# Kernel optimization log

Hardware: AMD Instinct MI355X
Metric: run time of the kernel (lower is better)

The kernel has to match this reference:

```python
import jax, jax.numpy as jnp
import numpy as np
from itertools import permutations

D_DIA, L_DIA, N_DIM, NHID, NUM_K = 128, 40, 512, 512, 4
N_UTT = D_DIA * L_DIA          # 5120 utterances
N_NODE = 3 * N_UTT             # 15360 graph nodes (l,a,v per utterance)


def _build_edges(n_dia, dia_l):
    """Replicates create_gnn_index edge construction for uniform dialogue length.
    Intra-modal: all ordered pairs within each modality block per dialogue.
    Cross-modal: ordered pairs among {l_t, a_t, v_t} for each utterance t."""
    base = (np.arange(n_dia) * 3 * dia_l).reshape(n_dia, 1, 1)
    p, q = np.meshgrid(np.arange(dia_l), np.arange(dia_l), indexing='ij')
    mask = p != q
    pp, qq = p[mask], q[mask]                      # [L*(L-1)]
    moff = (np.arange(3) * dia_l).reshape(1, 3, 1)  # modality block offsets
    src_i = (base + moff + pp.reshape(1, 1, -1)).ravel()
    dst_i = (base + moff + qq.reshape(1, 1, -1)).ravel()
    tri = np.array(list(permutations(range(3), 2)))  # [6,2]
    t = np.arange(dia_l).reshape(1, 1, -1)
    src_c = (base + tri[:, 0].reshape(1, 6, 1) * dia_l + t).ravel()
    dst_c = (base + tri[:, 1].reshape(1, 6, 1) * dia_l + t).ravel()
    src = np.concatenate([src_i, src_c]).astype(np.int32)
    dst = np.concatenate([dst_i, dst_c]).astype(np.int32)
    return jnp.asarray(src), jnp.asarray(dst)


def setup_inputs() -> dict:
    key = jax.random.key(0)
    ks = jax.random.split(key, 10)
    a = jax.random.normal(ks[0], (N_UTT, N_DIM), jnp.float32)
    v = jax.random.normal(ks[1], (N_UTT, N_DIM), jnp.float32)
    l = jax.random.normal(ks[2], (N_UTT, N_DIM), jnp.float32)
    qmask = jax.random.uniform(ks[3], (L_DIA, D_DIA, 2), jnp.float32)
    dia_len = jnp.full((D_DIA,), L_DIA, jnp.int32)
    spk_emb = jax.random.normal(ks[4], (2, N_DIM), jnp.float32)
    fc1_W = jax.random.normal(ks[5], (N_DIM, NHID), jnp.float32) / np.sqrt(N_DIM)
    fc1_b = jnp.zeros((NHID,), jnp.float32)
    convW = jax.random.normal(ks[6], (NUM_K, NHID, NHID), jnp.float32) / np.sqrt(NHID)
    convb = jnp.zeros((NUM_K, NHID), jnp.float32)
    src, dst = _build_edges(D_DIA, L_DIA)
    return {"a": a, "v": v, "l": l, "qmask": qmask, "spk_emb": spk_emb,
            "fc1_W": fc1_W, "fc1_b": fc1_b, "convW": convW, "convb": convb,
            "dia_len": dia_len, "epoch": 0, "src": src, "dst": dst}


def _gcn_conv(x, src, dst, W, b):
    # GCNConv: D^{-1/2}(A+I)D^{-1/2} X W + b, scatter-add aggregation over edges
    n = x.shape[0]
    deg = jax.ops.segment_sum(jnp.ones(src.shape[0], x.dtype), dst, num_segments=n) + 1.0
    norm = jax.lax.rsqrt(deg)
    coef = norm[src] * norm[dst]                       # [E]
    agg = jax.ops.segment_sum(x[src] * coef[:, None], dst, num_segments=n)
    agg = agg + x / deg[:, None]                       # self-loop term
    return agg @ W + b


def reference(a, v, l, qmask, spk_emb, fc1_W, fc1_b, convW, convb, dia_len, epoch, src, dst):
    n_dia = dia_len.shape[0]
    ll = L_DIA
    # speaker embedding added to text modality (use_speaker=True, 'l' in modals)
    spk_idx = jnp.argmax(qmask[:ll].transpose(1, 0, 2).reshape(-1, qmask.shape[-1]), axis=-1)
    l = l + spk_emb[spk_idx]
    # node features ordered per dialogue as [l_block, a_block, v_block]
    feats = jnp.concatenate([l.reshape(n_dia, ll, -1),
                             a.reshape(n_dia, ll, -1),
                             v.reshape(n_dia, ll, -1)], axis=1).reshape(3 * n_dia * ll, -1)
    x1 = feats @ fc1_W + fc1_b
    gnn_out = x1
    for k in range(convW.shape[0]):
        gnn_out = gnn_out + _gcn_conv(gnn_out, src, dst, convW[k], convb[k])
    out2 = jnp.concatenate([x1, gnn_out], axis=1)
    out2 = jnp.concatenate([feats, out2], axis=-1)     # use_residue=True
    # reverse_features: regroup per dialogue, concat modalities on feature dim
    d2 = out2.shape[-1]
    r = out2.reshape(n_dia, 3, ll, d2)
    out1 = jnp.concatenate([r[:, 0], r[:, 1], r[:, 2]], axis=-1).reshape(n_dia * ll, 3 * d2)
    return out1
```

## Files before the change

kernel.cpp:

```cpp
#include <hip/hip_runtime.h>
#include <cstdint>
#include <cstddef>

typedef unsigned short u16;
typedef __attribute__((ext_vector_type(8))) short bf16x8;
typedef __attribute__((ext_vector_type(4))) float f32x4;

__device__ __forceinline__ float b2f(u16 u) {
  union { uint32_t i; float f; } x; x.i = ((uint32_t)u) << 16; return x.f;
}
__device__ __forceinline__ u16 f2b(float f) {
  union { float f; uint32_t i; } x; x.f = f;
  uint32_t u = x.i;
  u += 0x7fffu + ((u >> 16) & 1u);
  return (u16)(u >> 16);
}
__device__ __forceinline__ void load8(const void* p, size_t idx, bool f32, float o[8]) {
  if (f32) {
    const float4* fp = (const float4*)((const float*)p + idx);
    float4 x = fp[0], y = fp[1];
    o[0] = x.x; o[1] = x.y; o[2] = x.z; o[3] = x.w;
    o[4] = y.x; o[5] = y.y; o[6] = y.z; o[7] = y.w;
  } else {
    uint4 w = *(const uint4*)((const u16*)p + idx);
    uint32_t ww[4] = {w.x, w.y, w.z, w.w};
#pragma unroll
    for (int q = 0; q < 4; q++) {
      o[2 * q]     = b2f((u16)(ww[q] & 0xffffu));
      o[2 * q + 1] = b2f((u16)(ww[q] >> 16));
    }
  }
}
__device__ __forceinline__ void store8_bf16(u16* p, size_t idx, const float o[8]) {
  uint32_t w[4];
#pragma unroll
  for (int q = 0; q < 4; q++)
    w[q] = (uint32_t)f2b(o[2 * q]) | ((uint32_t)f2b(o[2 * q + 1]) << 16);
  *(uint4*)(p + idx) = make_uint4(w[0], w[1], w[2], w[3]);
}

__device__ __forceinline__ bool detect_f32(const u16* lb, int* ldsflag, int tid) {
  if (tid < 64) {
    int bad = 0;
    for (int i = tid; i < 1024; i += 64) {
      float f = b2f(lb[i]);
      if (!(fabsf(f) <= 1.0e4f)) bad = 1;
    }
    int any = __any(bad);
    if (tid == 0) *ldsflag = any;
  }
  __syncthreads();
  const bool r = (*ldsflag != 0);
  __syncthreads();
  return r;
}


__global__ __launch_bounds__(1024)
void transw_k(const void* __restrict__ fc1W, const void* __restrict__ convW,
              const u16* __restrict__ lbits, u16* __restrict__ WtF)
{
  __shared__ u16 tile[32][33];
  __shared__ int flagS;
  const int tx = threadIdx.x, ty = threadIdx.y;
  const int tid = ty * 32 + tx;
  const bool f32 = detect_f32(lbits, &flagS, tid);
  const int w = blockIdx.z;
  const void* W = (w == 0) ? fc1W : convW;
  const size_t base = (w == 0) ? 0 : (size_t)(w - 1) * 262144;
  const int bx = blockIdx.x, by = blockIdx.y;
  const size_t i = base + (size_t)(by * 32 + ty) * 512 + (bx * 32 + tx);
  float val = f32 ? ((const float*)W)[i] : b2f(((const u16*)W)[i]);
  tile[ty][tx] = f2b(val);
  __syncthreads();
  const int e = tid & 7, l16 = (tid >> 3) & 15, q = (tid >> 7) & 3, nbp = tid >> 9;
  const u16 vv = tile[q * 8 + e][nbp * 16 + l16];
  WtF[(size_t)w * 262144 + ((size_t)((bx * 2 + nbp) * 16 + by)) * 512 +
      (q * 16 + l16) * 8 + e] = vv;
}


__device__ __forceinline__ void gemm_layer(f32x4 (&acc)[8][4], const u16* Xs,
                                           const u16* __restrict__ WL,
                                           int nt, int lane)
{
  const int lane8 = lane * 8;
  bf16x8 cw[4], nw[4];
#pragma unroll
  for (int nb = 0; nb < 4; ++nb)
    cw[nb] = *(const bf16x8*)(WL + (((nt * 4 + nb) * 16) << 9) + lane8);
#pragma unroll 2
  for (int kb = 0; kb < 16; ++kb) {
    if (kb < 15) {
#pragma unroll
      for (int nb = 0; nb < 4; ++nb)
        nw[nb] = *(const bf16x8*)(WL + (((nt * 4 + nb) * 16 + kb + 1) << 9) + lane8);
    }
    bf16x8 af[4];
#pragma unroll
    for (int rb = 0; rb < 4; ++rb)
      af[rb] = *(const bf16x8*)&Xs[((rb * 16 + kb) << 9) + lane8];
    __builtin_amdgcn_s_setprio(1);
#pragma unroll
    for (int rb = 0; rb < 4; ++rb)
#pragma unroll
      for (int nb = 0; nb < 4; ++nb)
        acc[rb][nb] = __builtin_amdgcn_mfma_f32_16x16x32_bf16(af[rb], cw[nb],
                                                              acc[rb][nb], 0, 0, 0);
    __builtin_amdgcn_s_setprio(0);
#pragma unroll
    for (int rb = 4; rb < 8; ++rb)
      af[rb - 4] = *(const bf16x8*)&Xs[((rb * 16 + kb) << 9) + lane8];
    __builtin_amdgcn_s_setprio(1);
#pragma unroll
    for (int rb = 4; rb < 8; ++rb)
#pragma unroll
      for (int nb = 0; nb < 4; ++nb)
        acc[rb][nb] = __builtin_amdgcn_mfma_f32_16x16x32_bf16(af[rb - 4], cw[nb],
                                                              acc[rb][nb], 0, 0, 0);
    __builtin_amdgcn_s_setprio(0);
#pragma unroll
    for (int nb = 0; nb < 4; ++nb) cw[nb] = nw[nb];
  }
}

__device__ __forceinline__ void bias_add(f32x4 (&acc)[8][4], const void* bptr,
                                         int boff, bool f32io, int nt, int l16)
{
#pragma unroll
  for (int nb = 0; nb < 4; ++nb) {
    const int col = nt * 64 + nb * 16 + l16;
    const float b = f32io ? ((const float*)bptr)[boff + col]
                          : b2f(((const u16*)bptr)[boff + col]);
#pragma unroll
    for (int rb = 0; rb < 8; ++rb)
#pragma unroll
      for (int r = 0; r < 4; ++r) acc[rb][nb][r] += b;
  }
}

__device__ __forceinline__ void writeout_co(void* outv, const f32x4 (&acc)[8][4],
                                            float* S, int d, int cbase, bool f32io,
                                            int nt, int quad, int l16, int tid)
{
  const int rg = tid >> 6;
  const int cs = (tid & 63) * 8;
#pragma unroll
  for (int p = 0; p < 3; ++p) {
    const int p0 = p * 40;
    __syncthreads();
#pragma unroll
    for (int rb = 0; rb < 8; ++rb)
#pragma unroll
      for (int r = 0; r < 4; ++r) {
        const int row = rb * 16 + quad * 4 + r;
        const int lr = row - p0;
        if (lr >= 0 && lr < 40) {
#pragma unroll
          for (int nb = 0; nb < 4; ++nb)
            S[lr * 516 + nt * 64 + nb * 16 + l16] = acc[rb][nb][r];
        }
      }
    __syncthreads();
#pragma unroll
    for (int it = 0; it < 5; ++it) {
      const int lr = it * 8 + rg;
      const size_t ob = (size_t)(d * 40 + lr) * 4608 + (size_t)p * 1536 + cbase + cs;
      const float* sp = &S[lr * 516 + cs];
      if (f32io) {
        float4 v0 = *(const float4*)sp, v1 = *(const float4*)(sp + 4);
        float* op = (float*)outv + ob;
        *(float4*)op = v0; *(float4*)(op + 4) = v1;
      } else {
        float vals[8];
#pragma unroll
        for (int q2 = 0; q2 < 8; ++q2) vals[q2] = sp[q2];
        store8_bf16((u16*)outv, ob, vals);
      }
    }
  }
}

__device__ __forceinline__ void gb_agg(const f32x4 (&acc)[8][4], u16* Xs,
                                       int nt, int lane, int quad, int l16)
{
#pragma unroll
  for (int nb = 0; nb < 4; ++nb) {
    const int c = nt * 64 + nb * 16 + l16;
    const int kc = c >> 5, cq = (c >> 3) & 3, e = c & 7;
#pragma unroll
    for (int rb = 0; rb < 8; ++rb)
#pragma unroll
      for (int r = 0; r < 4; ++r) {
        const int row = rb * 16 + quad * 4 + r;
        if (row < 120)
          Xs[((rb * 16 + kc) << 9) + (cq * 16 + (row & 15)) * 8 + e] =
              f2b(acc[rb][nb][r]);
      }
  }
  asm volatile("s_waitcnt lgkmcnt(0)" ::: "memory");
  const int c = nt * 64 + lane;
  const int kc = c >> 5, cq = (c >> 3) & 3, e = c & 7;
  float bs[3];
#pragma unroll
  for (int m = 0; m < 3; ++m) {
    float s = 0.f;
#pragma unroll 8
    for (int t = 0; t < 40; ++t) {
      const int row = m * 40 + t;
      s += b2f(Xs[(((row >> 4) * 16 + kc) << 9) + (cq * 16 + (row & 15)) * 8 + e]);
    }
    bs[m] = s;
  }
  const float inv42 = 1.0f / 42.0f;
#pragma unroll 4
  for (int t = 0; t < 40; ++t) {
    const int r0 = t, r1 = 40 + t, r2 = 80 + t;
    const int i0 = (((r0 >> 4) * 16 + kc) << 9) + (cq * 16 + (r0 & 15)) * 8 + e;
    const int i1 = (((r1 >> 4) * 16 + kc) << 9) + (cq * 16 + (r1 & 15)) * 8 + e;
    const int i2 = (((r2 >> 4) * 16 + kc) << 9) + (cq * 16 + (r2 & 15)) * 8 + e;
    const float x0 = b2f(Xs[i0]), x1 = b2f(Xs[i1]), x2 = b2f(Xs[i2]);
    Xs[i0] = f2b((bs[0] + x1 + x2) * inv42);
    Xs[i1] = f2b((bs[1] + x0 + x2) * inv42);
    Xs[i2] = f2b((bs[2] + x0 + x1) * inv42);
  }
}

__global__ __launch_bounds__(512, 2)
void fused_k(const void* __restrict__ a, const void* __restrict__ v,
             const void* __restrict__ l, const void* __restrict__ qmask,
             const void* __restrict__ spk, const void* __restrict__ fc1b,
             const void* __restrict__ convb, const u16* __restrict__ WtF,
             void* __restrict__ outv)
{
  __shared__ __align__(16) u16 Xs[65536];
  __shared__ int flagS;
  const int tid = threadIdx.x;
  const bool f32io = detect_f32((const u16*)l, &flagS, tid);
  const int d = blockIdx.x;
  const int lane = tid & 63, nt = tid >> 6;
  const int quad = lane >> 4, l16 = lane & 15;

  {
    const int cs = (tid & 63) * 8;
    const int rg = tid >> 6;
    const int kc = cs >> 5, cq = (cs >> 3) & 3;
#pragma unroll
    for (int it = 0; it < 15; ++it) {
      const int r = it * 8 + rg;
      const int mod = r / 40, t = r - mod * 40;
      const int u = d * 40 + t;
      float vals[8];
      const void* srcp = (mod == 1) ? a : ((mod == 2) ? v : l);
      load8(srcp, (size_t)u * 512 + cs, f32io, vals);
      if (mod == 0) {
        const int qi = (t * 128 + d) * 2;
        float q0 = f32io ? ((const float*)qmask)[qi]     : b2f(((const u16*)qmask)[qi]);
        float q1 = f32io ? ((const float*)qmask)[qi + 1] : b2f(((const u16*)qmask)[qi + 1]);
        const int sidx = (q1 > q0) ? 1 : 0;
        float sv[8];
        load8(spk, (size_t)sidx * 512 + cs, f32io, sv);
#pragma unroll
        for (int j = 0; j < 8; ++j) vals[j] += sv[j];
      }
      const size_t oidx = (size_t)u * 4608 + (size_t)mod * 1536 + cs;
      if (f32io) {
        float4* op = (float4*)((float*)outv + oidx);
        op[0] = make_float4(vals[0], vals[1], vals[2], vals[3]);
        op[1] = make_float4(vals[4], vals[5], vals[6], vals[7]);
      } else {
        store8_bf16((u16*)outv, oidx, vals);
      }
      uint32_t w[4];
#pragma unroll
      for (int p = 0; p < 4; ++p)
        w[p] = (uint32_t)f2b(vals[2 * p]) | ((uint32_t)f2b(vals[2 * p + 1]) << 16);
      *(uint4*)&Xs[(((r >> 4) * 16 + kc) << 9) + (cq * 16 + (r & 15)) * 8] =
          make_uint4(w[0], w[1], w[2], w[3]);
    }
    const int rz = 120 + rg;
    *(uint4*)&Xs[(((rz >> 4) * 16 + kc) << 9) + (cq * 16 + (rz & 15)) * 8] =
        make_uint4(0, 0, 0, 0);
  }
  __syncthreads();

  f32x4 acc[8][4];
#pragma unroll
  for (int rb = 0; rb < 8; ++rb)
#pragma unroll
    for (int nb = 0; nb < 4; ++nb) {
      f32x4 z = {0.f, 0.f, 0.f, 0.f};
      acc[rb][nb] = z;
    }
  gemm_layer(acc, Xs, WtF, nt, lane);
  bias_add(acc, fc1b, 0, f32io, nt, l16);
  writeout_co(outv, acc, (float*)Xs, d, 512, f32io, nt, quad, l16, tid);

#pragma unroll 1
  for (int L = 0; L < 4; ++L) {
    __syncthreads();
    gb_agg(acc, Xs, nt, lane, quad, l16);
    __syncthreads();
    gemm_layer(acc, Xs, WtF + (size_t)(L + 1) * 262144, nt, lane);
    bias_add(acc, convb, L * 512, f32io, nt, l16);
  }
  writeout_co(outv, acc, (float*)Xs, d, 1024, f32io, nt, quad, l16, tid);
}

extern "C" void kernel_launch(void* const* d_in, const int* in_sizes, int n_in,
                              void* d_out, int out_size, void* d_ws, size_t ws_size,
                              hipStream_t stream)
{
  const void* a     = d_in[0];
  const void* v     = d_in[1];
  const void* l     = d_in[2];
  const void* qmask = d_in[3];
  const void* spk   = d_in[4];
  const void* fc1W  = d_in[5];
  const void* fc1b  = d_in[6];
  const void* convW = d_in[7];
  const void* convb = d_in[8];

  u16* WtF = (u16*)d_ws;

  transw_k<<<dim3(16, 16, 5), dim3(32, 32), 0, stream>>>(fc1W, convW,
                                                         (const u16*)l, WtF);

  fused_k<<<128, 512, 0, stream>>>(a, v, l, qmask, spk, fc1b, convb, WtF, d_out);
}
```

Measured before the change: 262.6 us.

## Swizzle LDS tile layout, vectorize graph aggregation, and double-prefetch weights

The LDS activation tile now uses an XOR swizzle on the 16-byte group index to cut bank conflicts in the MFMA operand loads and scatter writes. The per-dialogue aggregation is split into two phases. Column sums are computed in registers with wave shuffles while bf16 values are written, and stored to a small LDS buffer. A vectorized update pass then processes 8 columns per thread using 128-bit LDS accesses. The weight prefetch in the GEMM goes two k-steps ahead and the k-loop is fully unrolled, which adds register pressure and an extra barrier per layer.

```diff
diff --git a/kernel.cpp b/kernel.cpp
--- a/kernel.cpp
+++ b/kernel.cpp
@@ -55,6 +55,9 @@
   return r;
 }
 
+__device__ __forceinline__ int xsw(int chunk, int G) {
+  return (chunk << 9) + (((G) ^ (chunk & 7)) << 3);
+}
 
 __global__ __launch_bounds__(1024)
 void transw_k(const void* __restrict__ fc1W, const void* __restrict__ convW,
@@ -79,48 +82,50 @@
       (q * 16 + l16) * 8 + e] = vv;
 }
 
-
 __device__ __forceinline__ void gemm_layer(f32x4 (&acc)[8][4], const u16* Xs,
                                            const u16* __restrict__ WL,
                                            int nt, int lane)
 {
   const int lane8 = lane * 8;
-  bf16x8 cw[4], nw[4];
-#pragma unroll
-  for (int nb = 0; nb < 4; ++nb)
-    cw[nb] = *(const bf16x8*)(WL + (((nt * 4 + nb) * 16) << 9) + lane8);
-#pragma unroll 2
+  bf16x8 w0[4], w1[4];
+#pragma unroll
+  for (int nb = 0; nb < 4; ++nb) {
+    w0[nb] = *(const bf16x8*)(WL + (((nt * 4 + nb) * 16 + 0) << 9) + lane8);
+    w1[nb] = *(const bf16x8*)(WL + (((nt * 4 + nb) * 16 + 1) << 9) + lane8);
+  }
+#pragma unroll
   for (int kb = 0; kb < 16; ++kb) {
-    if (kb < 15) {
+    bf16x8 w2[4];
+    if (kb < 14) {
 #pragma unroll
       for (int nb = 0; nb < 4; ++nb)
-        nw[nb] = *(const bf16x8*)(WL + (((nt * 4 + nb) * 16 + kb + 1) << 9) + lane8);
+        w2[nb] = *(const bf16x8*)(WL + (((nt * 4 + nb) * 16 + kb + 2) << 9) + lane8);
     }
     bf16x8 af[4];
 #pragma unroll
     for (int rb = 0; rb < 4; ++rb)
-      af[rb] = *(const bf16x8*)&Xs[((rb * 16 + kb) << 9) + lane8];
+      af[rb] = *(const bf16x8*)&Xs[xsw(rb * 16 + kb, lane)];
     __builtin_amdgcn_s_setprio(1);
 #pragma unroll
     for (int rb = 0; rb < 4; ++rb)
 #pragma unroll
       for (int nb = 0; nb < 4; ++nb)
-        acc[rb][nb] = __builtin_amdgcn_mfma_f32_16x16x32_bf16(af[rb], cw[nb],
+        acc[rb][nb] = __builtin_amdgcn_mfma_f32_16x16x32_bf16(af[rb], w0[nb],
                                                               acc[rb][nb], 0, 0, 0);
     __builtin_amdgcn_s_setprio(0);
 #pragma unroll
-    for (int rb = 4; rb < 8; ++rb)
-      af[rb - 4] = *(const bf16x8*)&Xs[((rb * 16 + kb) << 9) + lane8];
+    for (int rb = 0; rb < 4; ++rb)
+      af[rb] = *(const bf16x8*)&Xs[xsw((rb + 4) * 16 + kb, lane)];
     __builtin_amdgcn_s_setprio(1);
 #pragma unroll
-    for (int rb = 4; rb < 8; ++rb)
+    for (int rb = 0; rb < 4; ++rb)
 #pragma unroll
       for (int nb = 0; nb < 4; ++nb)
-        acc[rb][nb] = __builtin_amdgcn_mfma_f32_16x16x32_bf16(af[rb - 4], cw[nb],
-                                                              acc[rb][nb], 0, 0, 0);
+        acc[rb + 4][nb] = __builtin_amdgcn_mfma_f32_16x16x32_bf16(af[rb], w0[nb],
+                                                                  acc[rb + 4][nb], 0, 0, 0);
     __builtin_amdgcn_s_setprio(0);
 #pragma unroll
-    for (int nb = 0; nb < 4; ++nb) cw[nb] = nw[nb];
+    for (int nb = 0; nb < 4; ++nb) { w0[nb] = w1[nb]; w1[nb] = w2[nb]; }
   }
 }
 
@@ -136,6 +141,97 @@
     for (int rb = 0; rb < 8; ++rb)
 #pragma unroll
       for (int r = 0; r < 4; ++r) acc[rb][nb][r] += b;
+  }
+}
+
+__device__ __forceinline__ void gb_write_colsum(const f32x4 (&acc)[8][4], u16* Xs,
+                                                float* Bs, int nt, int quad, int l16)
+{
+  float ps0[4], ps1[4], ps2[4];
+#pragma unroll
+  for (int nb = 0; nb < 4; ++nb) { ps0[nb] = 0.f; ps1[nb] = 0.f; ps2[nb] = 0.f; }
+#pragma unroll
+  for (int nb = 0; nb < 4; ++nb) {
+    const int c = nt * 64 + nb * 16 + l16;
+    const int kc = c >> 5, cq = (c >> 3) & 3, e = c & 7;
+#pragma unroll
+    for (int rb = 0; rb < 8; ++rb)
+#pragma unroll
+      for (int r = 0; r < 4; ++r) {
+        const int row = rb * 16 + quad * 4 + r;
+        if (row < 120) {
+          const u16 hb = f2b(acc[rb][nb][r]);
+          Xs[xsw(rb * 16 + kc, cq * 16 + quad * 4 + r) + e] = hb;
+          const float fv = b2f(hb);
+          if (row < 40)      ps0[nb] += fv;
+          else if (row < 80) ps1[nb] += fv;
+          else               ps2[nb] += fv;
+        }
+      }
+  }
+#pragma unroll
+  for (int nb = 0; nb < 4; ++nb) {
+    ps0[nb] += __shfl_xor(ps0[nb], 16); ps0[nb] += __shfl_xor(ps0[nb], 32);
+    ps1[nb] += __shfl_xor(ps1[nb], 16); ps1[nb] += __shfl_xor(ps1[nb], 32);
+    ps2[nb] += __shfl_xor(ps2[nb], 16); ps2[nb] += __shfl_xor(ps2[nb], 32);
+  }
+  if (quad < 3) {
+#pragma unroll
+    for (int nb = 0; nb < 4; ++nb) {
+      const float s = (quad == 0) ? ps0[nb] : ((quad == 1) ? ps1[nb] : ps2[nb]);
+      Bs[quad * 512 + nt * 64 + nb * 16 + l16] = s;
+    }
+  }
+}
+
+__device__ __forceinline__ void agg_update(u16* Xs, const float* Bs, int nt, int lane)
+{
+  const int kc = lane >> 2, cq = lane & 3;
+  const int c0 = kc * 32 + cq * 8;
+  float b0[8], b1[8], b2[8];
+  *(float4*)&b0[0] = *(const float4*)&Bs[c0];
+  *(float4*)&b0[4] = *(const float4*)&Bs[c0 + 4];
+  *(float4*)&b1[0] = *(const float4*)&Bs[512 + c0];
+  *(float4*)&b1[4] = *(const float4*)&Bs[512 + c0 + 4];
+  *(float4*)&b2[0] = *(const float4*)&Bs[1024 + c0];
+  *(float4*)&b2[4] = *(const float4*)&Bs[1024 + c0 + 4];
+  const float inv42 = 1.0f / 42.0f;
+#pragma unroll
+  for (int i = 0; i < 5; ++i) {
+    const int t = nt * 5 + i;
+    const int r1 = 40 + t, r2 = 80 + t;
+    const int i0 = xsw((t  >> 4) * 16 + kc, cq * 16 + (t  & 15));
+    const int i1 = xsw((r1 >> 4) * 16 + kc, cq * 16 + (r1 & 15));
+    const int i2 = xsw((r2 >> 4) * 16 + kc, cq * 16 + (r2 & 15));
+    uint4 u0 = *(const uint4*)&Xs[i0];
+    uint4 u1 = *(const uint4*)&Xs[i1];
+    uint4 u2 = *(const uint4*)&Xs[i2];
+    uint32_t a0[4] = {u0.x, u0.y, u0.z, u0.w};
+    uint32_t a1[4] = {u1.x, u1.y, u1.z, u1.w};
+    uint32_t a2[4] = {u2.x, u2.y, u2.z, u2.w};
+    float f0[8], f1[8], f2[8];
+#pragma unroll
+    for (int q = 0; q < 4; ++q) {
+      f0[2*q] = b2f((u16)(a0[q] & 0xffffu)); f0[2*q+1] = b2f((u16)(a0[q] >> 16));
+      f1[2*q] = b2f((u16)(a1[q] & 0xffffu)); f1[2*q+1] = b2f((u16)(a1[q] >> 16));
+      f2[2*q] = b2f((u16)(a2[q] & 0xffffu)); f2[2*q+1] = b2f((u16)(a2[q] >> 16));
+    }
+    uint32_t p0[4], p1[4], p2[4];
+#pragma unroll
+    for (int q = 0; q < 4; ++q) {
+      const float o0a = (b0[2*q]   + f1[2*q]   + f2[2*q])   * inv42;
+      const float o0b = (b0[2*q+1] + f1[2*q+1] + f2[2*q+1]) * inv42;
+      const float o1a = (b1[2*q]   + f0[2*q]   + f2[2*q])   * inv42;
+      const float o1b = (b1[2*q+1] + f0[2*q+1] + f2[2*q+1]) * inv42;
+      const float o2a = (b2[2*q]   + f0[2*q]   + f1[2*q])   * inv42;
+      const float o2b = (b2[2*q+1] + f0[2*q+1] + f1[2*q+1]) * inv42;
+      p0[q] = (uint32_t)f2b(o0a) | ((uint32_t)f2b(o0b) << 16);
+      p1[q] = (uint32_t)f2b(o1a) | ((uint32_t)f2b(o1b) << 16);
+      p2[q] = (uint32_t)f2b(o2a) | ((uint32_t)f2b(o2b) << 16);
+    }
+    *(uint4*)&Xs[i0] = make_uint4(p0[0], p0[1], p0[2], p0[3]);
+    *(uint4*)&Xs[i1] = make_uint4(p1[0], p1[1], p1[2], p1[3]);
+    *(uint4*)&Xs[i2] = make_uint4(p2[0], p2[1], p2[2], p2[3]);
   }
 }
 
@@ -181,51 +277,6 @@
   }
 }
 
-__device__ __forceinline__ void gb_agg(const f32x4 (&acc)[8][4], u16* Xs,
-                                       int nt, int lane, int quad, int l16)
-{
-#pragma unroll
-  for (int nb = 0; nb < 4; ++nb) {
-    const int c = nt * 64 + nb * 16 + l16;
-    const int kc = c >> 5, cq = (c >> 3) & 3, e = c & 7;
-#pragma unroll
-    for (int rb = 0; rb < 8; ++rb)
-#pragma unroll
-      for (int r = 0; r < 4; ++r) {
-        const int row = rb * 16 + quad * 4 + r;
-        if (row < 120)
-          Xs[((rb * 16 + kc) << 9) + (cq * 16 + (row & 15)) * 8 + e] =
-              f2b(acc[rb][nb][r]);
-      }
-  }
-  asm volatile("s_waitcnt lgkmcnt(0)" ::: "memory");
-  const int c = nt * 64 + lane;
-  const int kc = c >> 5, cq = (c >> 3) & 3, e = c & 7;
-  float bs[3];
-#pragma unroll
-  for (int m = 0; m < 3; ++m) {
-    float s = 0.f;
-#pragma unroll 8
-    for (int t = 0; t < 40; ++t) {
-      const int row = m * 40 + t;
-      s += b2f(Xs[(((row >> 4) * 16 + kc) << 9) + (cq * 16 + (row & 15)) * 8 + e]);
-    }
-    bs[m] = s;
-  }
-  const float inv42 = 1.0f / 42.0f;
-#pragma unroll 4
-  for (int t = 0; t < 40; ++t) {
-    const int r0 = t, r1 = 40 + t, r2 = 80 + t;
-    const int i0 = (((r0 >> 4) * 16 + kc) << 9) + (cq * 16 + (r0 & 15)) * 8 + e;
-    const int i1 = (((r1 >> 4) * 16 + kc) << 9) + (cq * 16 + (r1 & 15)) * 8 + e;
-    const int i2 = (((r2 >> 4) * 16 + kc) << 9) + (cq * 16 + (r2 & 15)) * 8 + e;
-    const float x0 = b2f(Xs[i0]), x1 = b2f(Xs[i1]), x2 = b2f(Xs[i2]);
-    Xs[i0] = f2b((bs[0] + x1 + x2) * inv42);
-    Xs[i1] = f2b((bs[1] + x0 + x2) * inv42);
-    Xs[i2] = f2b((bs[2] + x0 + x1) * inv42);
-  }
-}
-
 __global__ __launch_bounds__(512, 2)
 void fused_k(const void* __restrict__ a, const void* __restrict__ v,
              const void* __restrict__ l, const void* __restrict__ qmask,
@@ -234,6 +285,7 @@
              void* __restrict__ outv)
 {
   __shared__ __align__(16) u16 Xs[65536];
+  __shared__ __align__(16) float Bs[1536];
   __shared__ int flagS;
   const int tid = threadIdx.x;
   const bool f32io = detect_f32((const u16*)l, &flagS, tid);
@@ -244,7 +296,7 @@
   {
     const int cs = (tid & 63) * 8;
     const int rg = tid >> 6;
-    const int kc = cs >> 5, cq = (cs >> 3) & 3;
+    const int kcf = cs >> 5, cqf = (cs >> 3) & 3;
 #pragma unroll
     for (int it = 0; it < 15; ++it) {
       const int r = it * 8 + rg;
@@ -275,11 +327,11 @@
 #pragma unroll
       for (int p = 0; p < 4; ++p)
         w[p] = (uint32_t)f2b(vals[2 * p]) | ((uint32_t)f2b(vals[2 * p + 1]) << 16);
-      *(uint4*)&Xs[(((r >> 4) * 16 + kc) << 9) + (cq * 16 + (r & 15)) * 8] =
+      *(uint4*)&Xs[xsw((r >> 4) * 16 + kcf, cqf * 16 + (r & 15))] =
           make_uint4(w[0], w[1], w[2], w[3]);
     }
     const int rz = 120 + rg;
-    *(uint4*)&Xs[(((rz >> 4) * 16 + kc) << 9) + (cq * 16 + (rz & 15)) * 8] =
+    *(uint4*)&Xs[xsw((rz >> 4) * 16 + kcf, cqf * 16 + (rz & 15))] =
         make_uint4(0, 0, 0, 0);
   }
   __syncthreads();
@@ -299,7 +351,9 @@
 #pragma unroll 1
   for (int L = 0; L < 4; ++L) {
     __syncthreads();
-    gb_agg(acc, Xs, nt, lane, quad, l16);
+    gb_write_colsum(acc, Xs, Bs, nt, quad, l16);
+    __syncthreads();
+    agg_update(Xs, Bs, nt, lane);
     __syncthreads();
     gemm_layer(acc, Xs, WtF + (size_t)(L + 1) * 262144, nt, lane);
     bias_add(acc, convb, L * 512, f32io, nt, l16);
```

Result: slower. 269.0 us (+2.4%).
